# Kernel optimization log

Measured on AMD Instinct MI355X. Metric: run time of the kernel, lower is better.

The kernel has to match this reference:

```python
import jax, jax.numpy as jnp
import numpy as np

V, H, O = 10000, 512, 512
B, S = 256, 256

def _xavier(key, shape):
    fan_in, fan_out = shape[1], shape[0]
    a = float(np.sqrt(6.0 / (fan_in + fan_out)))
    return jax.random.uniform(key, shape, jnp.float32, -a, a)

def setup_inputs() -> dict:
    key = jax.random.key(0)
    ks = jax.random.split(key, 8)
    x = jax.random.randint(ks[0], (B, S), 0, V)
    emb = _xavier(ks[1], (V, H))
    Wg = _xavier(ks[2], (2 * H, 2 * H))   # gates: in 2H -> out 2H (update|reset)
    bg = jnp.zeros((2 * H,), jnp.float32)
    Wh = _xavier(ks[3], (H, 2 * H))       # hidden_transform: in 2H -> out H
    bh = jnp.zeros((H,), jnp.float32)
    Wo = _xavier(ks[4], (O, H))           # out: in H -> out O
    bo = jnp.zeros((O,), jnp.float32)
    return {"x": x, "emb": emb, "Wg": Wg, "bg": bg, "Wh": Wh, "bh": bh, "Wo": Wo, "bo": bo}

def reference(x, emb, Wg, bg, Wh, bh, Wo, bo):
    xe = emb[x]                                  # [B,S,H]
    h0 = jnp.zeros((x.shape[0], H), emb.dtype)

    def step(h, xt):                              # xt: [B,H]
        g = jnp.concatenate([xt, h], axis=-1) @ Wg.T + bg   # [B,2H]
        z, r = jnp.split(jax.nn.sigmoid(g), 2, axis=-1)     # update, reset
        cand = jnp.tanh(jnp.concatenate([xt, r * h], axis=-1) @ Wh.T + bh)
        h_new = (1.0 - z) * h + z * cand
        y = h_new @ Wo.T + bo                    # [B,O]
        return h_new, y

    h_final, ys = jax.lax.scan(step, h0, jnp.swapaxes(xe, 0, 1))  # ys: [S,B,O]
    return h_final, jnp.swapaxes(ys, 0, 1)
```

## Files before the change

kernel.cpp:

```cpp
#include <hip/hip_runtime.h>
#include <math.h>

#define NB   256
#define NT   512
#define Bsz  256
#define Ssz  256
#define Hsz  512
#define Osz  512
#define RSTRIDE 1032

#define AGENT __HIP_MEMORY_SCOPE_AGENT
#define RLX   __ATOMIC_RELAXED

extern __shared__ float sx[];

__device__ __forceinline__ void stage_h(const float* src, int b0, int tid) {
  const int r = tid >> 4, l = tid & 15;
  const float* rowp = src + (((size_t)(b0 + r)) << 9);
  #pragma unroll
  for (int hh = 0; hh < 2; ++hh) {
    unsigned long long v0[4], v1[4];
    #pragma unroll
    for (int m = 0; m < 4; ++m) {
      const int g = ((hh << 2) + m) * 16 + l;
      v0[m] = __hip_atomic_load((const unsigned long long*)(rowp + (g << 2)), RLX, AGENT);
      v1[m] = __hip_atomic_load((const unsigned long long*)(rowp + (g << 2) + 2), RLX, AGENT);
    }
    #pragma unroll
    for (int m = 0; m < 4; ++m) {
      const int g = ((hh << 2) + m) * 16 + l;
      float* d = &sx[r * RSTRIDE + 512 + (g << 2)];
      *(unsigned long long*)d       = v0[m];
      *(unsigned long long*)(d + 2) = v1[m];
    }
  }
}

__device__ __forceinline__ void group_barrier(unsigned* flags, unsigned& target,
                                              int gbase, int tid, int bid) {
  ++target;
  __builtin_amdgcn_s_waitcnt(0);
  __syncthreads();
  __atomic_signal_fence(__ATOMIC_SEQ_CST);
  if (tid == 0)
    __hip_atomic_store(&flags[bid], target, RLX, AGENT);
  if (tid < 32) {
    while (__hip_atomic_load(&flags[gbase + tid], RLX, AGENT) < target)
      __builtin_amdgcn_s_sleep(2);
  }
  __atomic_signal_fence(__ATOMIC_SEQ_CST);
  __syncthreads();
}

__device__ __forceinline__ float reduce2(float acc0, float acc1, int ks) {
  float u = (ks & 1) ? acc1 : acc0;
  float v = (ks & 1) ? acc0 : acc1;
  u += __shfl_xor(v, 1);
  u += __shfl_xor(u, 2);
  u += __shfl_xor(u, 4);
  u += __shfl_xor(u, 8);
  u += __shfl_xor(u, 16);
  return u;
}

__global__ __attribute__((amdgpu_flat_work_group_size(NT, NT),
                          amdgpu_waves_per_eu(2, 2)))
void gru_persistent(
    const int* __restrict__ x, const float* __restrict__ emb,
    const float* __restrict__ Wg, const float* __restrict__ bgp,
    const float* __restrict__ Wh, const float* __restrict__ bhp,
    const float* __restrict__ Wo, const float* __restrict__ bop,
    float* __restrict__ out, float* __restrict__ ws)
{
  const int tid  = threadIdx.x;
  const int bid  = blockIdx.x;
  const int bgrp = bid >> 5;
  const int jg   = bid & 31;
  const int gbase = bgrp << 5;
  const int b0   = bgrp << 5;
  const int jp   = tid >> 5;
  const int ks   = tid & 31;
  const bool is_cand = (jg < 16);
  const int j0a = jg << 5;
  const int j0b = (jg & 15) << 5;
  const int jc0 = jp << 1;

  unsigned* flags = (unsigned*)ws;
  float* H0 = ws + 256;
  float* H1 = H0 + Bsz * Hsz;
  float* RH = H1 + Bsz * Hsz;
  float* ys = out + Bsz * Hsz;

  __shared__ float szv[32][32];
  __shared__ float shv[32][32];
  __shared__ int   sIdxN[32];

  float4 wa0[8], wa1[8];
  {
    const float* p0 = Wg + (size_t)(j0a + jc0) * 1024 + (ks << 2);
    const float* p1 = p0 + 1024;
    #pragma unroll
    for (int i = 0; i < 8; ++i) {
      wa0[i] = *(const float4*)(p0 + (i << 7));
      wa1[i] = *(const float4*)(p1 + (i << 7));
    }
  }
  float4 wb0[8], wb1[8];
  if (is_cand) {
    const float* p0 = Wh + (size_t)(j0b + jc0) * 1024 + (ks << 2);
    const float* p1 = p0 + 1024;
    #pragma unroll
    for (int i = 0; i < 8; ++i) {
      wb0[i] = *(const float4*)(p0 + (i << 7));
      wb1[i] = *(const float4*)(p1 + (i << 7));
    }
  } else {
    const float* p0 = Wo + (size_t)(j0b + jc0) * 512 + (ks << 2);
    const float* p1 = p0 + 512;
    #pragma unroll
    for (int i = 0; i < 4; ++i) {
      wb0[i] = *(const float4*)(p0 + (i << 7));
      wb1[i] = *(const float4*)(p1 + (i << 7));
    }
    #pragma unroll
    for (int i = 4; i < 8; ++i) {
      wb0[i] = make_float4(0.f, 0.f, 0.f, 0.f);
      wb1[i] = make_float4(0.f, 0.f, 0.f, 0.f);
    }
  }
  const float bA = bgp[j0a + jc0 + (ks & 1)];
  const float bB = is_cand ? bhp[j0b + jc0 + (ks & 1)] : bop[j0b + jc0 + (ks & 1)];

  const int pr = tid >> 4, pl = tid & 15;
  float4 xv[8];

  if (tid < 32) sIdxN[tid] = x[(b0 + tid) * Ssz];
  __syncthreads();
  {
    const float4* ep = (const float4*)(emb + (size_t)sIdxN[pr] * Hsz);
    #pragma unroll
    for (int m = 0; m < 8; ++m) xv[m] = ep[(m << 4) + pl];
  }

  unsigned target = 0;

  for (int t = 0; t < Ssz; ++t) {
    float* Hc = (t & 1) ? H1 : H0;
    float* Hn = (t & 1) ? H0 : H1;

    #pragma unroll
    for (int m = 0; m < 8; ++m)
      *(float4*)&sx[pr * RSTRIDE + (((m << 4) + pl) << 2)] = xv[m];
    stage_h(Hc, b0, tid);
    __syncthreads();

    if (tid < 32)
      sIdxN[tid] = x[(b0 + tid) * Ssz + ((t + 1 < Ssz) ? t + 1 : t)];

    {
      const int bx = ks << 2;
      #pragma unroll 2
      for (int r = 0; r < 32; ++r) {
        const float* xp = &sx[r * RSTRIDE + bx];
        float p00 = 0.f, p01 = 0.f, p02 = 0.f, p03 = 0.f;
        float p10 = 0.f, p11 = 0.f, p12 = 0.f, p13 = 0.f;
        #pragma unroll
        for (int i = 0; i < 8; ++i) {
          const float4 xq = *(const float4*)(xp + (i << 7));
          p00 += wa0[i].x * xq.x; p01 += wa0[i].y * xq.y;
          p02 += wa0[i].z * xq.z; p03 += wa0[i].w * xq.w;
          p10 += wa1[i].x * xq.x; p11 += wa1[i].y * xq.y;
          p12 += wa1[i].z * xq.z; p13 += wa1[i].w * xq.w;
        }
        const float u = reduce2((p00 + p01) + (p02 + p03),
                                (p10 + p11) + (p12 + p13), ks);
        if (ks < 2) {
          const int jj = jc0 + ks;
          const float s = 1.f / (1.f + expf(-(u + bA)));
          if (is_cand) {
            szv[r][jj] = s;
            shv[r][jj] = sx[r * RSTRIDE + 512 + j0b + jj];
          } else {
            const int hj = j0a + jj - 512;
            const float hv = sx[r * RSTRIDE + 512 + hj];
            __hip_atomic_store(RH + (((size_t)(b0 + r)) << 9) + hj, s * hv, RLX, AGENT);
          }
        }
      }
    }

    {
      ++target;
      __builtin_amdgcn_s_waitcnt(0);
      __syncthreads();
      __atomic_signal_fence(__ATOMIC_SEQ_CST);
      if (tid == 0)
        __hip_atomic_store(&flags[bid], target, RLX, AGENT);
      {
        const float4* ep = (const float4*)(emb + (size_t)sIdxN[pr] * Hsz);
        #pragma unroll
        for (int m = 0; m < 8; ++m) xv[m] = ep[(m << 4) + pl];
      }
      if (tid < 32) {
        while (__hip_atomic_load(&flags[gbase + tid], RLX, AGENT) < target)
          __builtin_amdgcn_s_sleep(2);
      }
      __atomic_signal_fence(__ATOMIC_SEQ_CST);
      __syncthreads();
    }

    if (is_cand) {
      stage_h(RH, b0, tid);
      __syncthreads();
      const int bx = ks << 2;
      #pragma unroll 2
      for (int r = 0; r < 32; ++r) {
        const float* xp = &sx[r * RSTRIDE + bx];
        float p00 = 0.f, p01 = 0.f, p02 = 0.f, p03 = 0.f;
        float p10 = 0.f, p11 = 0.f, p12 = 0.f, p13 = 0.f;
        #pragma unroll
        for (int i = 0; i < 8; ++i) {
          const float4 xq = *(const float4*)(xp + (i << 7));
          p00 += wb0[i].x * xq.x; p01 += wb0[i].y * xq.y;
          p02 += wb0[i].z * xq.z; p03 += wb0[i].w * xq.w;
          p10 += wb1[i].x * xq.x; p11 += wb1[i].y * xq.y;
          p12 += wb1[i].z * xq.z; p13 += wb1[i].w * xq.w;
        }
        const float u = reduce2((p00 + p01) + (p02 + p03),
                                (p10 + p11) + (p12 + p13), ks);
        if (ks < 2) {
          const int jj = jc0 + ks;
          const float cd = tanhf(u + bB);
          const float zv = szv[r][jj], hv = shv[r][jj];
          const float hn = (1.f - zv) * hv + zv * cd;
          __hip_atomic_store(Hn + (((size_t)(b0 + r)) << 9) + (j0b + jj), hn, RLX, AGENT);
          if (t == Ssz - 1) out[((b0 + r) << 9) + (j0b + jj)] = hn;
        }
      }
    } else if (t > 0) {
      const int bx = 512 + (ks << 2);
      #pragma unroll 2
      for (int r = 0; r < 32; ++r) {
        const float* xp = &sx[r * RSTRIDE + bx];
        float p00 = 0.f, p01 = 0.f, p02 = 0.f, p03 = 0.f;
        float p10 = 0.f, p11 = 0.f, p12 = 0.f, p13 = 0.f;
        #pragma unroll
        for (int i = 0; i < 4; ++i) {
          const float4 xq = *(const float4*)(xp + (i << 7));
          p00 += wb0[i].x * xq.x; p01 += wb0[i].y * xq.y;
          p02 += wb0[i].z * xq.z; p03 += wb0[i].w * xq.w;
          p10 += wb1[i].x * xq.x; p11 += wb1[i].y * xq.y;
          p12 += wb1[i].z * xq.z; p13 += wb1[i].w * xq.w;
        }
        const float u = reduce2((p00 + p01) + (p02 + p03),
                                (p10 + p11) + (p12 + p13), ks);
        if (ks < 2)
          ys[((size_t)(b0 + r) * Ssz + (t - 1)) * Osz + (j0b + jc0 + ks)] = u + bB;
      }
    }

    group_barrier(flags, target, gbase, tid, bid);
  }

  if (!is_cand) {
    stage_h(H0, b0, tid);
    __syncthreads();
    const int bx = 512 + (ks << 2);
    #pragma unroll 2
    for (int r = 0; r < 32; ++r) {
      const float* xp = &sx[r * RSTRIDE + bx];
      float p00 = 0.f, p01 = 0.f, p02 = 0.f, p03 = 0.f;
      float p10 = 0.f, p11 = 0.f, p12 = 0.f, p13 = 0.f;
      #pragma unroll
      for (int i = 0; i < 4; ++i) {
        const float4 xq = *(const float4*)(xp + (i << 7));
        p00 += wb0[i].x * xq.x; p01 += wb0[i].y * xq.y;
        p02 += wb0[i].z * xq.z; p03 += wb0[i].w * xq.w;
        p10 += wb1[i].x * xq.x; p11 += wb1[i].y * xq.y;
        p12 += wb1[i].z * xq.z; p13 += wb1[i].w * xq.w;
      }
      const float u = reduce2((p00 + p01) + (p02 + p03),
                              (p10 + p11) + (p12 + p13), ks);
      if (ks < 2)
        ys[((size_t)(b0 + r) * Ssz + (Ssz - 1)) * Osz + (j0b + jc0 + ks)] = u + bB;
    }
  }
}

extern "C" void kernel_launch(void* const* d_in, const int* in_sizes, int n_in,
                              void* d_out, int out_size, void* d_ws, size_t ws_size,
                              hipStream_t stream) {
  const int*   x   = (const int*)  d_in[0];
  const float* emb = (const float*)d_in[1];
  const float* Wg  = (const float*)d_in[2];
  const float* bg  = (const float*)d_in[3];
  const float* Wh  = (const float*)d_in[4];
  const float* bh  = (const float*)d_in[5];
  const float* Wo  = (const float*)d_in[6];
  const float* bo  = (const float*)d_in[7];
  float* out = (float*)d_out;
  float* ws  = (float*)d_ws;

  const int dynLds = 32 * RSTRIDE * 4;
  hipFuncSetAttribute((const void*)gru_persistent,
                      hipFuncAttributeMaxDynamicSharedMemorySize, dynLds);

  hipMemsetAsync(d_ws, 0, (256 + Bsz * Hsz) * sizeof(float), stream);

  gru_persistent<<<NB, NT, dynLds, stream>>>(x, emb, Wg, bg, Wh, bh, Wo, bo, out, ws);
}
```

Measured before the change: 10.50 ms.

## Remap work to full 64-lane waves with four outputs each and vectorized stores

Each 64-lane wavefront now computes four output columns over the full K dimension instead of 32-lane groups computing two columns, so each LDS load of the input row is reused across four weight rows and the butterfly reduction covers the whole wave. Per-element atomic stores of r*h and the new hidden state are replaced by staging in shared memory and coalesced 64-bit atomic stores after a block sync. The aim is fewer LDS reads per FMA and fewer global transactions per step, at the cost of an extra __syncthreads and a deeper shuffle reduction.

```diff
diff --git a/kernel.cpp b/kernel.cpp
--- a/kernel.cpp
+++ b/kernel.cpp
@@ -11,6 +11,7 @@
 
 #define AGENT __HIP_MEMORY_SCOPE_AGENT
 #define RLX   __ATOMIC_RELAXED
+typedef unsigned long long ull_t;
 
 extern __shared__ float sx[];
 
@@ -19,19 +20,19 @@
   const float* rowp = src + (((size_t)(b0 + r)) << 9);
   #pragma unroll
   for (int hh = 0; hh < 2; ++hh) {
-    unsigned long long v0[4], v1[4];
+    ull_t v0[4], v1[4];
     #pragma unroll
     for (int m = 0; m < 4; ++m) {
       const int g = ((hh << 2) + m) * 16 + l;
-      v0[m] = __hip_atomic_load((const unsigned long long*)(rowp + (g << 2)), RLX, AGENT);
-      v1[m] = __hip_atomic_load((const unsigned long long*)(rowp + (g << 2) + 2), RLX, AGENT);
+      v0[m] = __hip_atomic_load((const ull_t*)(rowp + (g << 2)), RLX, AGENT);
+      v1[m] = __hip_atomic_load((const ull_t*)(rowp + (g << 2) + 2), RLX, AGENT);
     }
     #pragma unroll
     for (int m = 0; m < 4; ++m) {
       const int g = ((hh << 2) + m) * 16 + l;
       float* d = &sx[r * RSTRIDE + 512 + (g << 2)];
-      *(unsigned long long*)d       = v0[m];
-      *(unsigned long long*)(d + 2) = v1[m];
+      *(ull_t*)d       = v0[m];
+      *(ull_t*)(d + 2) = v1[m];
     }
   }
 }
@@ -52,14 +53,21 @@
   __syncthreads();
 }
 
-__device__ __forceinline__ float reduce2(float acc0, float acc1, int ks) {
-  float u = (ks & 1) ? acc1 : acc0;
-  float v = (ks & 1) ? acc0 : acc1;
-  u += __shfl_xor(v, 1);
-  u += __shfl_xor(u, 2);
+__device__ __forceinline__ float reduce4(float a0, float a1, float a2, float a3,
+                                         int ks) {
+  float u01 = (ks & 1) ? a1 : a0;
+  float v01 = (ks & 1) ? a0 : a1;
+  u01 += __shfl_xor(v01, 1);
+  float u23 = (ks & 1) ? a3 : a2;
+  float v23 = (ks & 1) ? a2 : a3;
+  u23 += __shfl_xor(v23, 1);
+  float u = (ks & 2) ? u23 : u01;
+  float v = (ks & 2) ? u01 : u23;
+  u += __shfl_xor(v, 2);
   u += __shfl_xor(u, 4);
   u += __shfl_xor(u, 8);
   u += __shfl_xor(u, 16);
+  u += __shfl_xor(u, 32);
   return u;
 }
 
@@ -78,12 +86,12 @@
   const int jg   = bid & 31;
   const int gbase = bgrp << 5;
   const int b0   = bgrp << 5;
-  const int jp   = tid >> 5;
-  const int ks   = tid & 31;
+  const int wv   = tid >> 6;
+  const int ks   = tid & 63;
   const bool is_cand = (jg < 16);
   const int j0a = jg << 5;
   const int j0b = (jg & 15) << 5;
-  const int jc0 = jp << 1;
+  const int jc0 = wv << 2;
 
   unsigned* flags = (unsigned*)ws;
   float* H0 = ws + 256;
@@ -93,43 +101,36 @@
 
   __shared__ float szv[32][32];
   __shared__ float shv[32][32];
+  __shared__ float sWB[32][32];
   __shared__ int   sIdxN[32];
 
-  float4 wa0[8], wa1[8];
+  float4 wa[4][4];
   {
-    const float* p0 = Wg + (size_t)(j0a + jc0) * 1024 + (ks << 2);
-    const float* p1 = p0 + 1024;
-    #pragma unroll
-    for (int i = 0; i < 8; ++i) {
-      wa0[i] = *(const float4*)(p0 + (i << 7));
-      wa1[i] = *(const float4*)(p1 + (i << 7));
-    }
-  }
-  float4 wb0[8], wb1[8];
+    const float* p = Wg + (size_t)(j0a + jc0) * 1024 + (ks << 2);
+    #pragma unroll
+    for (int c = 0; c < 4; ++c)
+      #pragma unroll
+      for (int i = 0; i < 4; ++i)
+        wa[c][i] = *(const float4*)(p + c * 1024 + (i << 8));
+  }
+  float4 wb[4][4];
   if (is_cand) {
-    const float* p0 = Wh + (size_t)(j0b + jc0) * 1024 + (ks << 2);
-    const float* p1 = p0 + 1024;
-    #pragma unroll
-    for (int i = 0; i < 8; ++i) {
-      wb0[i] = *(const float4*)(p0 + (i << 7));
-      wb1[i] = *(const float4*)(p1 + (i << 7));
-    }
+    const float* p = Wh + (size_t)(j0b + jc0) * 1024 + (ks << 2);
+    #pragma unroll
+    for (int c = 0; c < 4; ++c)
+      #pragma unroll
+      for (int i = 0; i < 4; ++i)
+        wb[c][i] = *(const float4*)(p + c * 1024 + (i << 8));
   } else {
-    const float* p0 = Wo + (size_t)(j0b + jc0) * 512 + (ks << 2);
-    const float* p1 = p0 + 512;
-    #pragma unroll
-    for (int i = 0; i < 4; ++i) {
-      wb0[i] = *(const float4*)(p0 + (i << 7));
-      wb1[i] = *(const float4*)(p1 + (i << 7));
-    }
-    #pragma unroll
-    for (int i = 4; i < 8; ++i) {
-      wb0[i] = make_float4(0.f, 0.f, 0.f, 0.f);
-      wb1[i] = make_float4(0.f, 0.f, 0.f, 0.f);
-    }
-  }
-  const float bA = bgp[j0a + jc0 + (ks & 1)];
-  const float bB = is_cand ? bhp[j0b + jc0 + (ks & 1)] : bop[j0b + jc0 + (ks & 1)];
+    const float* p = Wo + (size_t)(j0b + jc0) * 512 + (ks << 2);
+    #pragma unroll
+    for (int c = 0; c < 4; ++c)
+      #pragma unroll
+      for (int i = 0; i < 2; ++i)
+        wb[c][i] = *(const float4*)(p + c * 512 + (i << 8));
+  }
+  const float bA = bgp[j0a + jc0 + (ks & 3)];
+  const float bB = is_cand ? bhp[j0b + jc0 + (ks & 3)] : bop[j0b + jc0 + (ks & 3)];
 
   const int pr = tid >> 4, pl = tid & 15;
   float4 xv[8];
@@ -142,6 +143,7 @@
     for (int m = 0; m < 8; ++m) xv[m] = ep[(m << 4) + pl];
   }
 
+  const int bx = ks << 2;
   unsigned target = 0;
 
   for (int t = 0; t < Ssz; ++t) {
@@ -158,23 +160,28 @@
       sIdxN[tid] = x[(b0 + tid) * Ssz + ((t + 1 < Ssz) ? t + 1 : t)];
 
     {
-      const int bx = ks << 2;
       #pragma unroll 2
       for (int r = 0; r < 32; ++r) {
         const float* xp = &sx[r * RSTRIDE + bx];
-        float p00 = 0.f, p01 = 0.f, p02 = 0.f, p03 = 0.f;
-        float p10 = 0.f, p11 = 0.f, p12 = 0.f, p13 = 0.f;
+        float4 acc0 = {0.f,0.f,0.f,0.f}, acc1 = {0.f,0.f,0.f,0.f};
+        float4 acc2 = {0.f,0.f,0.f,0.f}, acc3 = {0.f,0.f,0.f,0.f};
         #pragma unroll
-        for (int i = 0; i < 8; ++i) {
-          const float4 xq = *(const float4*)(xp + (i << 7));
-          p00 += wa0[i].x * xq.x; p01 += wa0[i].y * xq.y;
-          p02 += wa0[i].z * xq.z; p03 += wa0[i].w * xq.w;
-          p10 += wa1[i].x * xq.x; p11 += wa1[i].y * xq.y;
-          p12 += wa1[i].z * xq.z; p13 += wa1[i].w * xq.w;
-        }
-        const float u = reduce2((p00 + p01) + (p02 + p03),
-                                (p10 + p11) + (p12 + p13), ks);
-        if (ks < 2) {
+        for (int i = 0; i < 4; ++i) {
+          const float4 xq = *(const float4*)(xp + (i << 8));
+          acc0.x += wa[0][i].x * xq.x; acc0.y += wa[0][i].y * xq.y;
+          acc0.z += wa[0][i].z * xq.z; acc0.w += wa[0][i].w * xq.w;
+          acc1.x += wa[1][i].x * xq.x; acc1.y += wa[1][i].y * xq.y;
+          acc1.z += wa[1][i].z * xq.z; acc1.w += wa[1][i].w * xq.w;
+          acc2.x += wa[2][i].x * xq.x; acc2.y += wa[2][i].y * xq.y;
+          acc2.z += wa[2][i].z * xq.z; acc2.w += wa[2][i].w * xq.w;
+          acc3.x += wa[3][i].x * xq.x; acc3.y += wa[3][i].y * xq.y;
+          acc3.z += wa[3][i].z * xq.z; acc3.w += wa[3][i].w * xq.w;
+        }
+        const float u = reduce4((acc0.x + acc0.y) + (acc0.z + acc0.w),
+                                (acc1.x + acc1.y) + (acc1.z + acc1.w),
+                                (acc2.x + acc2.y) + (acc2.z + acc2.w),
+                                (acc3.x + acc3.y) + (acc3.z + acc3.w), ks);
+        if (ks < 4) {
           const int jj = jc0 + ks;
           const float s = 1.f / (1.f + expf(-(u + bA)));
           if (is_cand) {
@@ -182,11 +189,18 @@
             shv[r][jj] = sx[r * RSTRIDE + 512 + j0b + jj];
           } else {
             const int hj = j0a + jj - 512;
-            const float hv = sx[r * RSTRIDE + 512 + hj];
-            __hip_atomic_store(RH + (((size_t)(b0 + r)) << 9) + hj, s * hv, RLX, AGENT);
+            sWB[r][jj] = s * sx[r * RSTRIDE + 512 + hj];
           }
         }
       }
+    }
+
+    __syncthreads();
+    if (!is_cand) {
+      const int row = tid >> 4, q = tid & 15;
+      __hip_atomic_store(
+          (ull_t*)(RH + (((size_t)(b0 + row)) << 9) + (j0a - 512) + (q << 1)),
+          *(const ull_t*)&sWB[row][q << 1], RLX, AGENT);
     }
 
     {
@@ -212,49 +226,68 @@
     if (is_cand) {
       stage_h(RH, b0, tid);
       __syncthreads();
-      const int bx = ks << 2;
       #pragma unroll 2
       for (int r = 0; r < 32; ++r) {
         const float* xp = &sx[r * RSTRIDE + bx];
-        float p00 = 0.f, p01 = 0.f, p02 = 0.f, p03 = 0.f;
-        float p10 = 0.f, p11 = 0.f, p12 = 0.f, p13 = 0.f;
+        float4 acc0 = {0.f,0.f,0.f,0.f}, acc1 = {0.f,0.f,0.f,0.f};
+        float4 acc2 = {0.f,0.f,0.f,0.f}, acc3 = {0.f,0.f,0.f,0.f};
         #pragma unroll
-        for (int i = 0; i < 8; ++i) {
-          const float4 xq = *(const float4*)(xp + (i << 7));
-          p00 += wb0[i].x * xq.x; p01 += wb0[i].y * xq.y;
-          p02 += wb0[i].z * xq.z; p03 += wb0[i].w * xq.w;
-          p10 += wb1[i].x * xq.x; p11 += wb1[i].y * xq.y;
-          p12 += wb1[i].z * xq.z; p13 += wb1[i].w * xq.w;
-        }
-        const float u = reduce2((p00 + p01) + (p02 + p03),
-                                (p10 + p11) + (p12 + p13), ks);
-        if (ks < 2) {
+        for (int i = 0; i < 4; ++i) {
+          const float4 xq = *(const float4*)(xp + (i << 8));
+          acc0.x += wb[0][i].x * xq.x; acc0.y += wb[0][i].y * xq.y;
+          acc0.z += wb[0][i].z * xq.z; acc0.w += wb[0][i].w * xq.w;
+          acc1.x += wb[1][i].x * xq.x; acc1.y += wb[1][i].y * xq.y;
+          acc1.z += wb[1][i].z * xq.z; acc1.w += wb[1][i].w * xq.w;
+          acc2.x += wb[2][i].x * xq.x; acc2.y += wb[2][i].y * xq.y;
+          acc2.z += wb[2][i].z * xq.z; acc2.w += wb[2][i].w * xq.w;
+          acc3.x += wb[3][i].x * xq.x; acc3.y += wb[3][i].y * xq.y;
+          acc3.z += wb[3][i].z * xq.z; acc3.w += wb[3][i].w * xq.w;
+        }
+        const float u = reduce4((acc0.x + acc0.y) + (acc0.z + acc0.w),
+                                (acc1.x + acc1.y) + (acc1.z + acc1.w),
+                                (acc2.x + acc2.y) + (acc2.z + acc2.w),
+                                (acc3.x + acc3.y) + (acc3.z + acc3.w), ks);
+        if (ks < 4) {
           const int jj = jc0 + ks;
           const float cd = tanhf(u + bB);
           const float zv = szv[r][jj], hv = shv[r][jj];
-          const float hn = (1.f - zv) * hv + zv * cd;
-          __hip_atomic_store(Hn + (((size_t)(b0 + r)) << 9) + (j0b + jj), hn, RLX, AGENT);
-          if (t == Ssz - 1) out[((b0 + r) << 9) + (j0b + jj)] = hn;
-        }
+          sWB[r][jj] = (1.f - zv) * hv + zv * cd;
+        }
+      }
+      __syncthreads();
+      {
+        const int row = tid >> 4, q = tid & 15;
+        const ull_t v = *(const ull_t*)&sWB[row][q << 1];
+        __hip_atomic_store(
+            (ull_t*)(Hn + (((size_t)(b0 + row)) << 9) + j0b + (q << 1)),
+            v, RLX, AGENT);
+        if (t == Ssz - 1)
+          *(ull_t*)(out + (((b0 + row)) << 9) + j0b + (q << 1)) = v;
       }
     } else if (t > 0) {
-      const int bx = 512 + (ks << 2);
+      const int by = 512 + bx;
       #pragma unroll 2
       for (int r = 0; r < 32; ++r) {
-        const float* xp = &sx[r * RSTRIDE + bx];
-        float p00 = 0.f, p01 = 0.f, p02 = 0.f, p03 = 0.f;
-        float p10 = 0.f, p11 = 0.f, p12 = 0.f, p13 = 0.f;
+        const float* xp = &sx[r * RSTRIDE + by];
+        float4 acc0 = {0.f,0.f,0.f,0.f}, acc1 = {0.f,0.f,0.f,0.f};
+        float4 acc2 = {0.f,0.f,0.f,0.f}, acc3 = {0.f,0.f,0.f,0.f};
         #pragma unroll
-        for (int i = 0; i < 4; ++i) {
-          const float4 xq = *(const float4*)(xp + (i << 7));
-          p00 += wb0[i].x * xq.x; p01 += wb0[i].y * xq.y;
-          p02 += wb0[i].z * xq.z; p03 += wb0[i].w * xq.w;
-          p10 += wb1[i].x * xq.x; p11 += wb1[i].y * xq.y;
-          p12 += wb1[i].z * xq.z; p13 += wb1[i].w * xq.w;
-        }
-        const float u = reduce2((p00 + p01) + (p02 + p03),
-                                (p10 + p11) + (p12 + p13), ks);
-        if (ks < 2)
+        for (int i = 0; i < 2; ++i) {
+          const float4 xq = *(const float4*)(xp + (i << 8));
+          acc0.x += wb[0][i].x * xq.x; acc0.y += wb[0][i].y * xq.y;
+          acc0.z += wb[0][i].z * xq.z; acc0.w += wb[0][i].w * xq.w;
+          acc1.x += wb[1][i].x * xq.x; acc1.y += wb[1][i].y * xq.y;
+          acc1.z += wb[1][i].z * xq.z; acc1.w += wb[1][i].w * xq.w;
+          acc2.x += wb[2][i].x * xq.x; acc2.y += wb[2][i].y * xq.y;
+          acc2.z += wb[2][i].z * xq.z; acc2.w += wb[2][i].w * xq.w;
+          acc3.x += wb[3][i].x * xq.x; acc3.y += wb[3][i].y * xq.y;
+          acc3.z += wb[3][i].z * xq.z; acc3.w += wb[3][i].w * xq.w;
+        }
+        const float u = reduce4((acc0.x + acc0.y) + (acc0.z + acc0.w),
+                                (acc1.x + acc1.y) + (acc1.z + acc1.w),
+                                (acc2.x + acc2.y) + (acc2.z + acc2.w),
+                                (acc3.x + acc3.y) + (acc3.z + acc3.w), ks);
+        if (ks < 4)
           ys[((size_t)(b0 + r) * Ssz + (t - 1)) * Osz + (j0b + jc0 + ks)] = u + bB;
       }
     }
@@ -265,23 +298,29 @@
   if (!is_cand) {
     stage_h(H0, b0, tid);
     __syncthreads();
-    const int bx = 512 + (ks << 2);
+    const int by = 512 + bx;
     #pragma unroll 2
     for (int r = 0; r < 32; ++r) {
-      const float* xp = &sx[r * RSTRIDE + bx];
-      float p00 = 0.f, p01 = 0.f, p02 = 0.f, p03 = 0.f;
-      float p10 = 0.f, p11 = 0.f, p12 = 0.f, p13 = 0.f;
+      const float* xp = &sx[r * RSTRIDE + by];
+      float4 acc0 = {0.f,0.f,0.f,0.f}, acc1 = {0.f,0.f,0.f,0.f};
+      float4 acc2 = {0.f,0.f,0.f,0.f}, acc3 = {0.f,0.f,0.f,0.f};
       #pragma unroll
-      for (int i = 0; i < 4; ++i) {
-        const float4 xq = *(const float4*)(xp + (i << 7));
-        p00 += wb0[i].x * xq.x; p01 += wb0[i].y * xq.y;
-        p02 += wb0[i].z * xq.z; p03 += wb0[i].w * xq.w;
-        p10 += wb1[i].x * xq.x; p11 += wb1[i].y * xq.y;
-        p12 += wb1[i].z * xq.z; p13 += wb1[i].w * xq.w;
-      }
-      const float u = reduce2((p00 + p01) + (p02 + p03),
-                              (p10 + p11) + (p12 + p13), ks);
-      if (ks < 2)
+      for (int i = 0; i < 2; ++i) {
+        const float4 xq = *(const float4*)(xp + (i << 8));
+        acc0.x += wb[0][i].x * xq.x; acc0.y += wb[0][i].y * xq.y;
+        acc0.z += wb[0][i].z * xq.z; acc0.w += wb[0][i].w * xq.w;
+        acc1.x += wb[1][i].x * xq.x; acc1.y += wb[1][i].y * xq.y;
+        acc1.z += wb[1][i].z * xq.z; acc1.w += wb[1][i].w * xq.w;
+        acc2.x += wb[2][i].x * xq.x; acc2.y += wb[2][i].y * xq.y;
+        acc2.z += wb[2][i].z * xq.z; acc2.w += wb[2][i].w * xq.w;
+        acc3.x += wb[3][i].x * xq.x; acc3.y += wb[3][i].y * xq.y;
+        acc3.z += wb[3][i].z * xq.z; acc3.w += wb[3][i].w * xq.w;
+      }
+      const float u = reduce4((acc0.x + acc0.y) + (acc0.z + acc0.w),
+                              (acc1.x + acc1.y) + (acc1.z + acc1.w),
+                              (acc2.x + acc2.y) + (acc2.z + acc2.w),
+                              (acc3.x + acc3.y) + (acc3.z + acc3.w), ks);
+      if (ks < 4)
         ys[((size_t)(b0 + r) * Ssz + (Ssz - 1)) * Osz + (j0b + jc0 + ks)] = u + bB;
     }
   }
```

Result: slower. 11.05 ms (+5.2%).
